# Performance work log

Measured on AMD Instinct MI355X. Metric: run time of the kernel, lower is better.

Reference implementation:

```python
import jax, jax.numpy as jnp
import numpy as np

B, T_IN, T_OUT = 32, 512, 800
N_MEL, ENC, ARNN, DRNN, PRE, ATT, LOCF, LOCK = 80, 512, 1024, 1024, 256, 128, 32, 31


def setup_inputs() -> dict:
    key = jax.random.key(0)
    ks = jax.random.split(key, 24)
    s = 0.02
    d = {
        'memory': jax.random.normal(ks[0], (B, T_IN, ENC), jnp.float32),
        'decoder_inputs': jax.random.normal(ks[1], (B, N_MEL, T_OUT), jnp.float32),
        'prenet_w1': jax.random.normal(ks[2], (PRE, N_MEL)) * s,
        'prenet_w2': jax.random.normal(ks[3], (PRE, PRE)) * s,
        'att_rnn_wih': jax.random.normal(ks[4], (4 * ARNN, PRE + ENC)) * s,
        'att_rnn_whh': jax.random.normal(ks[5], (4 * ARNN, ARNN)) * s,
        'att_rnn_bih': jnp.zeros((4 * ARNN,)),
        'att_rnn_bhh': jnp.zeros((4 * ARNN,)),
        'q_w': jax.random.normal(ks[6], (ATT, ARNN)) * s,
        'mem_w': jax.random.normal(ks[7], (ATT, ENC)) * s,
        'v_w': jax.random.normal(ks[8], (1, ATT)) * s,
        'loc_conv_w': jax.random.normal(ks[9], (LOCF, 2, LOCK)) * s,
        'loc_lin_w': jax.random.normal(ks[10], (ATT, LOCF)) * s,
        'dec_rnn_wih': jax.random.normal(ks[11], (4 * DRNN, ARNN + ENC)) * s,
        'dec_rnn_whh': jax.random.normal(ks[12], (4 * DRNN, DRNN)) * s,
        'dec_rnn_bih': jnp.zeros((4 * DRNN,)),
        'dec_rnn_bhh': jnp.zeros((4 * DRNN,)),
        'proj_w': jax.random.normal(ks[13], (N_MEL, DRNN + ENC)) * s,
        'proj_b': jnp.zeros((N_MEL,)),
        'gate_w': jax.random.normal(ks[14], (1, DRNN + ENC)) * s,
        'gate_b': jnp.zeros((1,)),
    }
    lengths = jax.random.randint(ks[15], (B,), T_IN // 2, T_IN + 1)
    d['memory_lengths'] = lengths.at[0].set(T_IN)  # ensure max length spans memory
    return d


def _lstm_cell(x, h, c, wih, whh, bih, bhh):
    z = x @ wih.T + bih + h @ whh.T + bhh
    i, f, g, o = jnp.split(z, 4, axis=-1)
    c = jax.nn.sigmoid(f) * c + jax.nn.sigmoid(i) * jnp.tanh(g)
    h = jax.nn.sigmoid(o) * jnp.tanh(c)
    return h, c


def reference(memory, decoder_inputs, prenet_w1, prenet_w2,
              att_rnn_wih, att_rnn_whh, att_rnn_bih, att_rnn_bhh,
              q_w, mem_w, v_w, loc_conv_w, loc_lin_w,
              dec_rnn_wih, dec_rnn_whh, dec_rnn_bih, dec_rnn_bhh,
              proj_w, proj_b, gate_w, gate_b, memory_lengths):
    # teacher-forced inputs: go frame + first T_OUT-1 mel frames -> [T_OUT, B, N_MEL]
    frames = jnp.transpose(decoder_inputs, (2, 0, 1))  # [T_OUT, B, N_MEL]
    dec_in = jnp.concatenate([jnp.zeros((1, B, N_MEL), memory.dtype), frames[:-1]], 0)
    # prenet (dropout omitted for deterministic reference)
    x = jax.nn.relu(dec_in @ prenet_w1.T)
    pren = jax.nn.relu(x @ prenet_w2.T)  # [T_OUT, B, PRE]

    pmem = memory @ mem_w.T  # [B, T_IN, ATT]
    valid = jnp.arange(T_IN)[None, :] < memory_lengths[:, None]  # [B, T_IN]

    def step(carry, dec_t):
        ah, ac, dh, dc, aw, awc, actx = carry
        cell_in = jnp.concatenate([dec_t, actx], -1)
        ah, ac = _lstm_cell(cell_in, ah, ac, att_rnn_wih, att_rnn_whh, att_rnn_bih, att_rnn_bhh)
        # location-sensitive attention
        cat = jnp.stack([aw, awc], axis=1)  # [B, 2, T_IN]
        loc = jax.lax.conv_general_dilated(cat, loc_conv_w, (1,), 'SAME',
                                           dimension_numbers=('NCH', 'OIH', 'NCH'))  # [B, LOCF, T_IN]
        loc = jnp.einsum('bct,ac->bta', loc, loc_lin_w)  # [B, T_IN, ATT]
        pq = (ah @ q_w.T)[:, None, :]  # [B, 1, ATT]
        energies = jnp.einsum('bta,a->bt', jnp.tanh(pq + loc + pmem), v_w[0])
        energies = jnp.where(valid, energies, -1e9)
        aw = jax.nn.softmax(energies, axis=1)
        actx = jnp.einsum('bt,btd->bd', aw, memory)
        awc = awc + aw
        din = jnp.concatenate([ah, actx], -1)
        dh, dc = _lstm_cell(din, dh, dc, dec_rnn_wih, dec_rnn_whh, dec_rnn_bih, dec_rnn_bhh)
        dhac = jnp.concatenate([dh, actx], -1)
        mel = dhac @ proj_w.T + proj_b  # [B, N_MEL]
        gate = (dhac @ gate_w.T + gate_b)[:, 0]  # [B]
        return (ah, ac, dh, dc, aw, awc, actx), (mel, gate, aw)

    z = lambda *s: jnp.zeros(s, memory.dtype)
    carry0 = (z(B, ARNN), z(B, ARNN), z(B, DRNN), z(B, DRNN), z(B, T_IN), z(B, T_IN), z(B, ENC))
    _, (mels, gates, aligns) = jax.lax.scan(step, carry0, pren)
    mel_outputs = jnp.transpose(mels, (1, 2, 0))      # [B, N_MEL, T_OUT]
    gate_outputs = jnp.transpose(gates, (1, 0))       # [B, T_OUT]
    alignments = jnp.transpose(aligns, (1, 0, 2))     # [B, T_OUT, T_IN]
    return mel_outputs, gate_outputs, alignments
```

## Files before the change

### kernel.cpp

```cpp
#include <hip/hip_runtime.h>
#include <cstddef>


constexpr size_t WT_ATT = 0;
constexpr size_t WT_DEC = 7340032;
constexpr size_t PREN_O = 17825792;
constexpr size_t PMEMT  = 24379392;
constexpr size_t W1T    = 26476544;
constexpr size_t W2T    = 26497024;
constexpr size_t QWT    = 26562560;
constexpr size_t PWT    = 26693632;
constexpr size_t MEMWT  = 26841088;
constexpr size_t ZDEC0  = 26906624;
constexpr size_t ZDEC1  = 27037696;
constexpr size_t AH_O   = 27185152;
constexpr size_t AC_O   = 27217920;
constexpr size_t DH_O   = 27250688;
constexpr size_t DC_O   = 27283456;
constexpr size_t AWC_O  = 27316224;
constexpr size_t ACTX_O = 27348992;
constexpr size_t ENER_O = 27381760;
constexpr size_t LOC_O  = 27398144;
constexpr size_t BAR_O  = 27922432;

constexpr size_t MEL_OUT = 0;
constexpr size_t GATE_OUT = 2048000;
constexpr size_t ALIGN_OUT = 2073600;

__device__ __forceinline__ float* zatt_ptr(float* ws, int b) {
  return ws + (b < 21 ? (size_t)W1T + (size_t)b * 4096
                      : (size_t)MEMWT + (size_t)(b - 21) * 4096);
}

__device__ __forceinline__ float gload(const float* p_) {
  return __hip_atomic_load(p_, __ATOMIC_RELAXED, __HIP_MEMORY_SCOPE_AGENT);
}
__device__ __forceinline__ void gstore(float* p_, float v) {
  __hip_atomic_store(p_, v, __ATOMIC_RELAXED, __HIP_MEMORY_SCOPE_AGENT);
}

__device__ __forceinline__ void gsync(float* ws, unsigned& epoch) {
  unsigned* cnt = (unsigned*)(ws + BAR_O);
  unsigned* rel = (unsigned*)(ws + BAR_O) + 128;
  __syncthreads();
  const int tid = threadIdx.x, bid = blockIdx.x;
  ++epoch;
  if (tid == 0)
    __hip_atomic_fetch_add(&cnt[(bid & 31) * 4], 1u, __ATOMIC_RELAXED,
                           __HIP_MEMORY_SCOPE_AGENT);
  if (bid == 0) {
    if (tid < 64) {
      const unsigned tgt = epoch * 24u;
      bool done;
      do {
        unsigned v = (tid < 32) ? __hip_atomic_load(&cnt[tid * 4], __ATOMIC_RELAXED,
                                                    __HIP_MEMORY_SCOPE_AGENT)
                                : tgt;
        done = v >= tgt;
        if (!done) __builtin_amdgcn_s_sleep(2);
      } while (__ballot(done) != ~0ull);
      for (int rr = tid; rr < 768; rr += 64)
        __hip_atomic_store(&rel[rr * 4], epoch, __ATOMIC_RELAXED,
                           __HIP_MEMORY_SCOPE_AGENT);
    }
  } else if (tid == 0) {
    while (__hip_atomic_load(&rel[bid * 4], __ATOMIC_RELAXED,
                             __HIP_MEMORY_SCOPE_AGENT) < epoch)
      __builtin_amdgcn_s_sleep(4);
  }
  __syncthreads();
}

__device__ __forceinline__ float sigf(float x) {
  float cx = fminf(fmaxf(x, -30.f), 30.f);
  return 1.f / (1.f + __expf(-cx));
}
__device__ __forceinline__ float tanh_f(float x) {
  float cx = fminf(fmaxf(x, -15.f), 15.f);
  float e = __expf(2.f * cx);
  return (e - 1.f) / (e + 1.f);
}

__device__ __forceinline__ void fused2(
    float* __restrict__ ws,
    const float* __restrict__ XA, const int sA, const int ncA,
    const float* __restrict__ XB, const int sB,
    const int nc, const float* __restrict__ WB,
    const int mode, const int g, const int b0, const int t,
    const float* __restrict__ bih, const float* __restrict__ bhh,
    float* __restrict__ cst, float* __restrict__ d0,
    const int tid, float* __restrict__ sm) {
  float* Xs = sm;
  float* Ws = sm + 2560;
  const int cg = tid & 7, bg = (tid >> 3) & 1, ks = tid >> 4;
  float acc[4][8];
#pragma unroll
  for (int ci = 0; ci < 4; ++ci)
#pragma unroll
    for (int bi = 0; bi < 8; ++bi) acc[ci][bi] = 0.f;

  const int kloc = tid & 127, brow = tid >> 7;
  float px[8];
  float4 pw[4];
  {
#pragma unroll
    for (int i = 0; i < 8; ++i)
      px[i] = gload(XA + (size_t)(brow + 2 * i) * sA + kloc);
  }
#pragma unroll
  for (int j = 0; j < 4; ++j)
    pw[j] = *(const float4*)(WB + (size_t)tid * 4 + j * 1024);

#pragma unroll 1
  for (int c = 0; c < nc; ++c) {
    __syncthreads();
#pragma unroll
    for (int i = 0; i < 8; ++i) Xs[kloc * 20 + brow + 2 * i] = px[i];
#pragma unroll
    for (int j = 0; j < 4; ++j) {
      const int ff = tid + 256 * j;
      *(float4*)(Ws + (ff >> 3) * 36 + (ff & 7) * 4) = pw[j];
    }
    __syncthreads();
    if (c + 1 < nc) {
      const int c2 = c + 1;
      const bool inA = c2 < ncA;
      const float* base = inA ? XA : XB;
      const int st = inA ? sA : sB;
      const int ko = (inA ? c2 : c2 - ncA) * 128;
#pragma unroll
      for (int i = 0; i < 8; ++i)
        px[i] = gload(base + (size_t)(brow + 2 * i) * st + ko + kloc);
      const float* wb2 = WB + (size_t)c2 * 4096 + (size_t)tid * 4;
#pragma unroll
      for (int j = 0; j < 4; ++j) pw[j] = *(const float4*)(wb2 + j * 1024);
    }
#pragma unroll
    for (int i = 0; i < 8; ++i) {
      const int k = i * 16 + ks;
      const float4 wA = *(const float4*)(Ws + k * 36 + cg * 4);
      const float4 xA = *(const float4*)(Xs + k * 20 + bg * 8);
      const float4 xBv = *(const float4*)(Xs + k * 20 + bg * 8 + 4);
      const float wr[4] = {wA.x, wA.y, wA.z, wA.w};
      const float xr[8] = {xA.x, xA.y, xA.z, xA.w, xBv.x, xBv.y, xBv.z, xBv.w};
#pragma unroll
      for (int ci = 0; ci < 4; ++ci)
#pragma unroll
        for (int bi = 0; bi < 8; ++bi)
          acc[ci][bi] = fmaf(wr[ci], xr[bi], acc[ci][bi]);
    }
  }
#pragma unroll
  for (int ci = 0; ci < 4; ++ci)
#pragma unroll
    for (int bi = 0; bi < 8; ++bi) {
      float v = acc[ci][bi];
      v += __shfl_xor(v, 16);
      v += __shfl_xor(v, 32);
      acc[ci][bi] = v;
    }
  __syncthreads();
  float* red = sm;
  float* zs = sm + 2560;
  const int lane = tid & 63, wv = tid >> 6;
  if (lane < 16) {
#pragma unroll
    for (int ci = 0; ci < 4; ++ci)
#pragma unroll
      for (int bi = 0; bi < 8; ++bi)
        red[((bg * 8 + bi) * 32 + cg * 4 + ci) * 5 + wv] = acc[ci][bi];
  }
  __syncthreads();
#pragma unroll
  for (int m = 0; m < 2; ++m) {
    const int o = tid + 256 * m;
    zs[o] = red[o * 5] + red[o * 5 + 1] + red[o * 5 + 2] + red[o * 5 + 3];
  }
  __syncthreads();
  if (mode <= 2) {
#pragma unroll
    for (int m = 0; m < 2; ++m) {
      const int o = tid + 256 * m, bb = o >> 5, cp = o & 31, b = b0 + bb;
      float* dst = (mode == 2)
                       ? (zatt_ptr(ws, b) + (size_t)g * 32 + cp)
                       : (ws + (mode ? ZDEC1 : ZDEC0) + (size_t)b * 4096 +
                          (size_t)g * 32 + cp);
      gstore(dst, zs[o]);
    }
    return;
  }
  if (tid < 128) {
    const int bb = tid & 15, jj = tid >> 4;
    const int j = g * 8 + jj;
    const int b = b0 + bb;
    float za0 = 0.f, za1 = 0.f, za2 = 0.f, za3 = 0.f;
    if (mode == 3) {
      if (t > 0) {
        const float* zp = zatt_ptr(ws, b) + (size_t)g * 32 + jj;
        za0 = gload(zp);
        za1 = gload(zp + 8);
        za2 = gload(zp + 16);
        za3 = gload(zp + 24);
      }
    } else {
      const float* z0 = ws + ZDEC0 + (size_t)b * 4096 + (size_t)g * 32 + jj;
      const float* z1 = ws + ZDEC1 + (size_t)b * 4096 + (size_t)g * 32 + jj;
      za0 = gload(z0) + gload(z1);
      za1 = gload(z0 + 8) + gload(z1 + 8);
      za2 = gload(z0 + 16) + gload(z1 + 16);
      za3 = gload(z0 + 24) + gload(z1 + 24);
    }
    const float zi = zs[bb * 32 + jj] + za0 + bih[j] + bhh[j];
    const float zf = zs[bb * 32 + 8 + jj] + za1 + bih[1024 + j] + bhh[1024 + j];
    const float zg = zs[bb * 32 + 16 + jj] + za2 + bih[2048 + j] + bhh[2048 + j];
    const float zo = zs[bb * 32 + 24 + jj] + za3 + bih[3072 + j] + bhh[3072 + j];
    const float cp = cst[(size_t)b * 1024 + j];
    const float ct = sigf(zf) * cp + sigf(zi) * tanh_f(zg);
    const float ho = sigf(zo) * tanh_f(ct);
    cst[(size_t)b * 1024 + j] = ct;
    gstore(d0 + (size_t)b * 1024 + j, ho);
  }
}

__global__ __launch_bounds__(256) void k_small(
    const float* __restrict__ w1, const float* __restrict__ w2,
    const float* __restrict__ qw, const float* __restrict__ memw,
    const float* __restrict__ projw, const float* __restrict__ gatew,
    float* __restrict__ ws) {
  size_t i = (size_t)blockIdx.x * 256 + threadIdx.x;
  if (i < 20480) { size_t j = i & 255, m = i >> 8; ws[W1T + m * 256 + j] = w1[j * 80 + m]; return; }
  i -= 20480;
  if (i < 65536) { size_t j = i & 255, k = i >> 8; ws[W2T + k * 256 + j] = w2[j * 256 + k]; return; }
  i -= 65536;
  if (i < 131072) { size_t j = i & 127, k = i >> 7; ws[QWT + k * 128 + j] = qw[j * 1024 + k]; return; }
  i -= 131072;
  if (i < 65536) { size_t a = i & 127, e = i >> 7; ws[MEMWT + e * 128 + a] = memw[a * 512 + e]; return; }
  i -= 65536;
  if (i < 147456) {
    size_t o = i % 96, k = i / 96;
    float v = 0.f;
    if (o < 80) v = projw[o * 1536 + k];
    else if (o == 80) v = gatew[k];
    ws[PWT + k * 96 + o] = v;
  }
}

__device__ __forceinline__ size_t att_out(int gcol, int kout) {
  const int gate = gcol >> 10, g = (gcol & 1023) >> 3, jj = gcol & 7;
  return WT_ATT + ((size_t)g * 1792 + kout) * 32 + gate * 8 + jj;
}
__device__ __forceinline__ size_t dec_out(int gcol, int kout) {
  const int gate = gcol >> 10, g = (gcol & 1023) >> 3, jj = gcol & 7;
  return WT_DEC + ((size_t)g * 2560 + kout) * 32 + gate * 8 + jj;
}
__global__ __launch_bounds__(256) void k_tr_a_wih(const float* __restrict__ w,
                                                  float* __restrict__ ws) {
  const int i = blockIdx.x * 256 + threadIdx.x;
  const int gcol = i / 768, k = i - gcol * 768;
  ws[att_out(gcol, k)] = w[i];
}
__global__ __launch_bounds__(256) void k_tr_a_whh(const float* __restrict__ w,
                                                  float* __restrict__ ws) {
  const int i = blockIdx.x * 256 + threadIdx.x;
  const int gcol = i >> 10, kin = i & 1023;
  ws[att_out(gcol, 768 + kin)] = w[i];
}
__global__ __launch_bounds__(256) void k_tr_d_wih(const float* __restrict__ w,
                                                  float* __restrict__ ws) {
  const int i = blockIdx.x * 256 + threadIdx.x;
  const int gcol = i / 1536, kin = i - gcol * 1536;
  const int kout = (kin < 1024) ? kin : kin + 1024;
  ws[dec_out(gcol, kout)] = w[i];
}
__global__ __launch_bounds__(256) void k_tr_d_whh(const float* __restrict__ w,
                                                  float* __restrict__ ws) {
  const int i = blockIdx.x * 256 + threadIdx.x;
  const int gcol = i >> 10, kin = i & 1023;
  ws[dec_out(gcol, 1024 + kin)] = w[i];
}

__global__ __launch_bounds__(256) void k_prenet(const float* __restrict__ din,
                                                float* __restrict__ ws) {
  __shared__ float h1[8][257];
  const int tg = blockIdx.x, b = blockIdx.y, j = threadIdx.x;
  float acc[8] = {0, 0, 0, 0, 0, 0, 0, 0};
  for (int m = 0; m < 80; ++m) {
    const float w = ws[W1T + m * 256 + j];
#pragma unroll
    for (int q = 0; q < 8; ++q) {
      const int t = tg * 8 + q;
      const float x = (t > 0) ? din[((size_t)b * 80 + m) * 800 + (t - 1)] : 0.f;
      acc[q] = fmaf(x, w, acc[q]);
    }
  }
#pragma unroll
  for (int q = 0; q < 8; ++q) h1[q][j] = fmaxf(acc[q], 0.f);
  __syncthreads();
  float a2[8] = {0, 0, 0, 0, 0, 0, 0, 0};
  for (int k = 0; k < 256; ++k) {
    const float w = ws[W2T + k * 256 + j];
#pragma unroll
    for (int q = 0; q < 8; ++q) a2[q] = fmaf(h1[q][k], w, a2[q]);
  }
#pragma unroll
  for (int q = 0; q < 8; ++q) {
    const int t = tg * 8 + q;
    ws[PREN_O + ((size_t)t * 32 + b) * 256 + j] = fmaxf(a2[q], 0.f);
  }
}

__global__ __launch_bounds__(256) void k_pmem(const float* __restrict__ mem,
                                              float* __restrict__ ws) {
  __shared__ float mt[16 * 516];
  const int b = blockIdx.x, tc = blockIdx.y, tid = threadIdx.x;
  const int ti0 = tc * 16;
  for (int i = tid; i < 16 * 128; i += 256) {
    const int r = i >> 7, c = i & 127;
    *(float4*)(mt + r * 516 + c * 4) =
        *(const float4*)(mem + ((size_t)b * 512 + ti0 + r) * 512 + c * 4);
  }
  __syncthreads();
  const int a = tid & 127, th = tid >> 7;
  float acc[8] = {0, 0, 0, 0, 0, 0, 0, 0};
  for (int e = 0; e < 512; ++e) {
    const float w = ws[MEMWT + (size_t)e * 128 + a];
#pragma unroll
    for (int q = 0; q < 8; ++q) acc[q] = fmaf(w, mt[(th * 8 + q) * 516 + e], acc[q]);
  }
#pragma unroll
  for (int q = 0; q < 8; ++q)
    ws[PMEMT + ((size_t)b * 128 + a) * 512 + ti0 + th * 8 + q] = acc[q];
}

struct TP {
  const float *mem, *abih, *abhh, *lconv, *llw, *vw, *dbih, *dbhh, *projb, *gateb;
  const int* lens;
  float* ws;
  float* out;
};

__global__ __launch_bounds__(256, 3) void taco_main(TP p) {
  __shared__ float smem[7168];
  float* const ws = p.ws;
  unsigned epoch = 0;
  const int bid = blockIdx.x, tid = threadIdx.x;
  const int grp = bid >> 8, r = bid & 255;

#pragma unroll 1
  for (int t = 0; t <= 800; ++t) {
    const int par = t & 1, nxt = (t + 1) & 1, prv = (t - 1) & 1;
    if (grp == 0) {
      if (t < 800) {
        const int g = r >> 1, hh = r & 1, b0 = hh * 16;
        fused2(ws,
               ws + PREN_O + ((size_t)t * 32 + b0) * 256, 256, 2,
               ws + ACTX_O + (size_t)prv * 16384 + (size_t)b0 * 512, 512,
               6, ws + WT_ATT + (size_t)g * 1792 * 32,
               3, g, b0, t, p.abih, p.abhh, ws + AC_O, ws + AH_O,
               tid, smem);
      }
    } else if (grp == 1) {
      if (t > 0) {
        const int g = r >> 1, hh = r & 1, b0 = hh * 16;
        fused2(ws,
               ws + ACTX_O + (size_t)prv * 16384 + (size_t)b0 * 512, 512, 4,
               nullptr, 0,
               4, ws + WT_DEC + (size_t)g * 2560 * 32 + (size_t)2048 * 32,
               4, g, b0, t, p.dbih, p.dbhh, ws + DC_O, ws + DH_O,
               tid, smem);
      }
    }
    gsync(ws, epoch);

    if (t < 800) {
      if (grp == 0) {
        const int b = r >> 3, q8 = r & 7;
        float* sa = smem;
        float* sloc = smem + 1024;
        float* pqp = smem + 3136;
        float* pq = smem + 3392;
        float* sme = smem + 3520;
#pragma unroll
        for (int i = 0; i < 4; ++i)
          sa[tid + 256 * i] = gload(ws + AH_O + (size_t)b * 1024 + tid + 256 * i);
#pragma unroll
        for (int ii = 0; ii < 8; ++ii) {
          const int flat = tid + 256 * ii;
          sloc[(flat >> 5) * 33 + (flat & 31)] =
              gload(ws + LOC_O + (size_t)b * 16384 + (size_t)q8 * 2048 + flat);
        }
        __syncthreads();
        {
          const int j = tid & 127, kh = tid >> 7;
          const float* qb = ws + QWT + (size_t)kh * 512 * 128 + j;
          const float* ab = sa + kh * 512;
          float a0 = 0, a1 = 0, a2 = 0, a3 = 0;
          for (int k = 0; k < 512; k += 4) {
            a0 = fmaf(qb[(size_t)k * 128], ab[k], a0);
            a1 = fmaf(qb[(size_t)(k + 1) * 128], ab[k + 1], a1);
            a2 = fmaf(qb[(size_t)(k + 2) * 128], ab[k + 2], a2);
            a3 = fmaf(qb[(size_t)(k + 3) * 128], ab[k + 3], a3);
          }
          pqp[tid] = (a0 + a1) + (a2 + a3);
        }
        __syncthreads();
        if (tid < 128) pq[tid] = pqp[tid] + pqp[128 + tid];
        __syncthreads();
        const int ti_l = tid & 63, th = tid >> 6;
        float lr[32];
#pragma unroll
        for (int f = 0; f < 32; ++f) lr[f] = sloc[ti_l * 33 + f];
        const float* pmb = ws + PMEMT + (size_t)b * 65536 +
                           (size_t)(th * 32) * 512 + q8 * 64 + ti_l;
        float acc_e = 0;
#pragma unroll 2
        for (int a0 = 0; a0 < 32; ++a0) {
          const int a = th * 32 + a0;
          float s = pq[a] + pmb[(size_t)a0 * 512];
          const float* la = p.llw + a * 32;
#pragma unroll
          for (int f = 0; f < 32; ++f) s = fmaf(lr[f], la[f], s);
          acc_e = fmaf(p.vw[a], tanh_f(s), acc_e);
        }
        sme[tid] = acc_e;
        __syncthreads();
        if (tid < 64) {
          const int ti = q8 * 64 + tid;
          const float e = sme[tid] + sme[64 + tid] + sme[128 + tid] + sme[192 + tid];
          gstore(ws + ENER_O + (size_t)b * 512 + ti, (ti < p.lens[b]) ? e : -1e9f);
        }
      } else if (grp == 1) {
        const int g = r >> 1, hh = r & 1, b0 = hh * 16;
        fused2(ws, ws + AH_O + (size_t)b0 * 1024, 1024, 8, nullptr, 0, 8,
               ws + WT_DEC + (size_t)g * 2560 * 32,
               0, g, b0, t, nullptr, nullptr, nullptr, nullptr,
               tid, smem);
      } else {
        const int g = r >> 1, hh = r & 1, b0 = hh * 16;
        fused2(ws, ws + DH_O + (size_t)b0 * 1024, 1024, 8, nullptr, 0, 8,
               ws + WT_DEC + (size_t)g * 2560 * 32 + (size_t)1024 * 32,
               1, g, b0, t, nullptr, nullptr, nullptr, nullptr,
               tid, smem);
      }
    }
    gsync(ws, epoch);

    if (grp == 1 && t < 800) {
      const int b = r >> 3, dc8 = r & 7;
      float* se = smem;
      float* red = smem + 512;
      float* sp = smem + 768;
      float* sc = smem + 1280;
      float* saw = smem + 1536;
      float* sawh = smem + 1664;
      float* slc = smem + 1792;
      se[tid] = gload(ws + ENER_O + (size_t)b * 512 + tid);
      se[256 + tid] = gload(ws + ENER_O + (size_t)b * 512 + 256 + tid);
      for (int i = tid; i < 1984; i += 256) slc[i] = p.lconv[i];
      __syncthreads();
      red[tid] = fmaxf(se[tid], se[256 + tid]);
      __syncthreads();
      for (int s = 128; s > 0; s >>= 1) {
        if (tid < s) red[tid] = fmaxf(red[tid], red[tid + s]);
        __syncthreads();
      }
      const float mx = red[0];
      __syncthreads();
      const float p0 = __expf(se[tid] - mx), p1 = __expf(se[256 + tid] - mx);
      sp[tid] = p0;
      sp[256 + tid] = p1;
      red[tid] = p0 + p1;
      __syncthreads();
      for (int s = 128; s > 0; s >>= 1) {
        if (tid < s) red[tid] += red[tid + s];
        __syncthreads();
      }
      const float inv = 1.f / red[0];
      const int tseg = tid >> 6, dl = tid & 63;
      const int base = dc8 * 64;
      const float* mrow = p.mem + ((size_t)b * 512 + tseg * 128) * 512 + base + dl;
      float ca = 0, cb = 0;
      for (int i = 0; i < 128; i += 2) {
        ca = fmaf(sp[tseg * 128 + i], mrow[(size_t)i * 512], ca);
        cb = fmaf(sp[tseg * 128 + i + 1], mrow[(size_t)(i + 1) * 512], cb);
      }
      sc[tid] = ca + cb;
      for (int i = tid; i < 95; i += 256) {
        const int x = base - 15 + i;
        const bool ok = (unsigned)x < 512u;
        const float awx = ok ? sp[x] * inv : 0.f;
        saw[i] = awx;
        sawh[i] = awx + (ok ? gload(ws + AWC_O + (size_t)par * 16384 +
                                    (size_t)b * 512 + x)
                            : 0.f);
      }
      __syncthreads();
      if (tid < 64) {
        const float v = (sc[tid] + sc[64 + tid] + sc[128 + tid] + sc[192 + tid]) * inv;
        const int dd = base + tid;
        gstore(ws + ACTX_O + (size_t)par * 16384 + (size_t)b * 512 + dd, v);
        gstore(ws + AWC_O + (size_t)nxt * 16384 + (size_t)b * 512 + dd,
               sawh[15 + tid]);
        p.out[ALIGN_OUT + ((size_t)b * 800 + t) * 512 + dd] = sp[dd] * inv;
      }
      if (t + 1 < 800) {
        const int f = tid & 31, tig = tid >> 5;
#pragma unroll 1
        for (int tt = 0; tt < 8; ++tt) {
          const int til = tig + tt * 8;
          float a2 = 0;
#pragma unroll
          for (int k2 = 0; k2 < 31; ++k2) a2 = fmaf(saw[til + k2], slc[f * 62 + k2], a2);
#pragma unroll
          for (int k2 = 0; k2 < 31; ++k2)
            a2 = fmaf(sawh[til + k2], slc[f * 62 + 31 + k2], a2);
          gstore(ws + LOC_O + (size_t)b * 16384 + (size_t)(base + til) * 32 + f, a2);
        }
      }
    } else if (grp == 2 && t + 1 < 800) {
      const int g = r >> 1, hh = r & 1, b0 = hh * 16;
      fused2(ws, ws + AH_O + (size_t)b0 * 1024, 1024, 8, nullptr, 0, 8,
             ws + WT_ATT + (size_t)g * 1792 * 32 + (size_t)768 * 32,
             2, g, b0, t, nullptr, nullptr, nullptr, nullptr,
             tid, smem);
    } else if (grp == 0 && r < 32 && t > 0) {
      const int b = r;
      float* sx = smem;
      float* sred = smem + 1536;
#pragma unroll
      for (int i = 0; i < 6; ++i) {
        const int flat = tid + 256 * i;
        sx[flat] = (flat < 1024)
                       ? gload(ws + DH_O + (size_t)b * 1024 + flat)
                       : gload(ws + ACTX_O + (size_t)prv * 16384 + (size_t)b * 512 +
                               (flat - 1024));
      }
      __syncthreads();
      float p0 = 0.f, p1 = 0.f, p2 = 0.f, p3 = 0.f;
      const int o = tid / 3, ks2 = tid - o * 3;
      if (o < 81) {
        const float* wcol = ws + PWT + o;
        const int k0 = ks2 * 512;
        for (int k = k0; k < k0 + 512; k += 4) {
          p0 = fmaf(sx[k], wcol[(size_t)k * 96], p0);
          p1 = fmaf(sx[k + 1], wcol[(size_t)(k + 1) * 96], p1);
          p2 = fmaf(sx[k + 2], wcol[(size_t)(k + 2) * 96], p2);
          p3 = fmaf(sx[k + 3], wcol[(size_t)(k + 3) * 96], p3);
        }
      }
      sred[tid] = (p0 + p1) + (p2 + p3);
      __syncthreads();
      if (tid < 81) {
        float ssum = sred[tid * 3] + sred[tid * 3 + 1] + sred[tid * 3 + 2];
        ssum += (tid < 80) ? p.projb[tid] : p.gateb[0];
        if (tid < 80)
          p.out[MEL_OUT + ((size_t)b * 80 + tid) * 800 + (t - 1)] = ssum;
        else
          p.out[GATE_OUT + (size_t)b * 800 + (t - 1)] = ssum;
      }
    }
    gsync(ws, epoch);
  }
}

extern "C" void kernel_launch(void* const* d_in, const int* in_sizes, int n_in,
                              void* d_out, int out_size, void* d_ws, size_t ws_size,
                              hipStream_t stream) {
  (void)in_sizes; (void)n_in; (void)out_size; (void)ws_size;
  const float* mem = (const float*)d_in[0];
  const float* decin = (const float*)d_in[1];
  const float* w1 = (const float*)d_in[2];
  const float* w2 = (const float*)d_in[3];
  const float* awih = (const float*)d_in[4];
  const float* awhh = (const float*)d_in[5];
  const float* abih = (const float*)d_in[6];
  const float* abhh = (const float*)d_in[7];
  const float* qw = (const float*)d_in[8];
  const float* memw = (const float*)d_in[9];
  const float* vw = (const float*)d_in[10];
  const float* lconv = (const float*)d_in[11];
  const float* llw = (const float*)d_in[12];
  const float* dwih = (const float*)d_in[13];
  const float* dwhh = (const float*)d_in[14];
  const float* dbih = (const float*)d_in[15];
  const float* dbhh = (const float*)d_in[16];
  const float* projw = (const float*)d_in[17];
  const float* projb = (const float*)d_in[18];
  const float* gatew = (const float*)d_in[19];
  const float* gateb = (const float*)d_in[20];
  const int* lens = (const int*)d_in[21];
  float* ws = (float*)d_ws;
  float* out = (float*)d_out;

  hipMemsetAsync(ws + ZDEC0, 0, 278528 * sizeof(float), stream);
  hipMemsetAsync(ws + AH_O, 0, 737280 * sizeof(float), stream);
  hipMemsetAsync(ws + BAR_O, 0, 4224 * sizeof(unsigned), stream);

  k_small<<<1680, 256, 0, stream>>>(w1, w2, qw, memw, projw, gatew, ws);
  k_tr_a_wih<<<12288, 256, 0, stream>>>(awih, ws);
  k_tr_a_whh<<<16384, 256, 0, stream>>>(awhh, ws);
  k_tr_d_wih<<<24576, 256, 0, stream>>>(dwih, ws);
  k_tr_d_whh<<<16384, 256, 0, stream>>>(dwhh, ws);
  k_prenet<<<dim3(100, 32), 256, 0, stream>>>(decin, ws);
  k_pmem<<<dim3(32, 32), 256, 0, stream>>>(mem, ws);

  TP tp{mem, abih, abhh, lconv, llw, vw, dbih, dbhh, projb, gateb, lens, ws, out};
  taco_main<<<768, 256, 0, stream>>>(tp);
}
```

Measured before the change: 156.5 ms.

## Rebalance persistent kernel onto 512 blocks and split decoder Whh matvec

Shrinks the persistent grid from 768 to 512 blocks (launch bounds now 2 per SIMD) and redistributes work across the phases between grid barriers. The decoder hidden-state matvec is split into two halves: one runs alongside the energy computation and the other follows the softmax, accumulating into the same buffer. The mel/gate projection is now a two-way partial sum combined in the next phase. The aim is to balance per-phase load and use fewer blocks per barrier. The cost is extra global accumulation traffic and more work per block.

```diff
diff --git a/kernel.cpp b/kernel.cpp
--- a/kernel.cpp
+++ b/kernel.cpp
@@ -11,8 +11,9 @@
 constexpr size_t QWT    = 26562560;
 constexpr size_t PWT    = 26693632;
 constexpr size_t MEMWT  = 26841088;
-constexpr size_t ZDEC0  = 26906624;
-constexpr size_t ZDEC1  = 27037696;
+constexpr size_t ZDA_O  = 26906624;
+constexpr size_t ZDH_O  = 27037696;
+constexpr size_t PP_O   = 27168768;
 constexpr size_t AH_O   = 27185152;
 constexpr size_t AC_O   = 27217920;
 constexpr size_t DH_O   = 27250688;
@@ -46,25 +47,25 @@
   const int tid = threadIdx.x, bid = blockIdx.x;
   ++epoch;
   if (tid == 0)
-    __hip_atomic_fetch_add(&cnt[(bid & 31) * 4], 1u, __ATOMIC_RELAXED,
+    __hip_atomic_fetch_add(&cnt[(bid & 15) * 8], 1u, __ATOMIC_RELAXED,
                            __HIP_MEMORY_SCOPE_AGENT);
   if (bid == 0) {
     if (tid < 64) {
-      const unsigned tgt = epoch * 24u;
+      const unsigned tgt = epoch * 32u;
       bool done;
       do {
-        unsigned v = (tid < 32) ? __hip_atomic_load(&cnt[tid * 4], __ATOMIC_RELAXED,
+        unsigned v = (tid < 16) ? __hip_atomic_load(&cnt[tid * 8], __ATOMIC_RELAXED,
                                                     __HIP_MEMORY_SCOPE_AGENT)
                                 : tgt;
         done = v >= tgt;
         if (!done) __builtin_amdgcn_s_sleep(2);
       } while (__ballot(done) != ~0ull);
-      for (int rr = tid; rr < 768; rr += 64)
-        __hip_atomic_store(&rel[rr * 4], epoch, __ATOMIC_RELAXED,
+      for (int rr = tid; rr < 512; rr += 64)
+        __hip_atomic_store(&rel[rr * 8], epoch, __ATOMIC_RELAXED,
                            __HIP_MEMORY_SCOPE_AGENT);
     }
   } else if (tid == 0) {
-    while (__hip_atomic_load(&rel[bid * 4], __ATOMIC_RELAXED,
+    while (__hip_atomic_load(&rel[bid * 8], __ATOMIC_RELAXED,
                              __HIP_MEMORY_SCOPE_AGENT) < epoch)
       __builtin_amdgcn_s_sleep(4);
   }
@@ -177,15 +178,17 @@
     zs[o] = red[o * 5] + red[o * 5 + 1] + red[o * 5 + 2] + red[o * 5 + 3];
   }
   __syncthreads();
-  if (mode <= 2) {
+  if (mode <= 2 || mode == 5) {
 #pragma unroll
     for (int m = 0; m < 2; ++m) {
       const int o = tid + 256 * m, bb = o >> 5, cp = o & 31, b = b0 + bb;
-      float* dst = (mode == 2)
-                       ? (zatt_ptr(ws, b) + (size_t)g * 32 + cp)
-                       : (ws + (mode ? ZDEC1 : ZDEC0) + (size_t)b * 4096 +
-                          (size_t)g * 32 + cp);
-      gstore(dst, zs[o]);
+      float* dst;
+      if (mode == 2) dst = zatt_ptr(ws, b) + (size_t)g * 32 + cp;
+      else if (mode == 0) dst = ws + ZDA_O + (size_t)b * 4096 + (size_t)g * 32 + cp;
+      else dst = ws + ZDH_O + (size_t)b * 4096 + (size_t)g * 32 + cp;
+      float v = zs[o];
+      if (mode == 5) v += gload(dst);
+      gstore(dst, v);
     }
     return;
   }
@@ -203,8 +206,8 @@
         za3 = gload(zp + 24);
       }
     } else {
-      const float* z0 = ws + ZDEC0 + (size_t)b * 4096 + (size_t)g * 32 + jj;
-      const float* z1 = ws + ZDEC1 + (size_t)b * 4096 + (size_t)g * 32 + jj;
+      const float* z0 = ws + ZDA_O + (size_t)b * 4096 + (size_t)g * 32 + jj;
+      const float* z1 = ws + ZDH_O + (size_t)b * 4096 + (size_t)g * 32 + jj;
       za0 = gload(z0) + gload(z1);
       za1 = gload(z0 + 8) + gload(z1 + 8);
       za2 = gload(z0 + 16) + gload(z1 + 16);
@@ -339,19 +342,18 @@
   float* out;
 };
 
-__global__ __launch_bounds__(256, 3) void taco_main(TP p) {
+__global__ __launch_bounds__(256, 2) void taco_main(TP p) {
   __shared__ float smem[7168];
   float* const ws = p.ws;
   unsigned epoch = 0;
   const int bid = blockIdx.x, tid = threadIdx.x;
-  const int grp = bid >> 8, r = bid & 255;
 
 #pragma unroll 1
   for (int t = 0; t <= 800; ++t) {
     const int par = t & 1, nxt = (t + 1) & 1, prv = (t - 1) & 1;
-    if (grp == 0) {
+    if (bid < 256) {
       if (t < 800) {
-        const int g = r >> 1, hh = r & 1, b0 = hh * 16;
+        const int g = bid >> 1, b0 = (bid & 1) * 16;
         fused2(ws,
                ws + PREN_O + ((size_t)t * 32 + b0) * 256, 256, 2,
                ws + ACTX_O + (size_t)prv * 16384 + (size_t)b0 * 512, 512,
@@ -359,9 +361,9 @@
                3, g, b0, t, p.abih, p.abhh, ws + AC_O, ws + AH_O,
                tid, smem);
       }
-    } else if (grp == 1) {
+    } else {
       if (t > 0) {
-        const int g = r >> 1, hh = r & 1, b0 = hh * 16;
+        const int rd = bid - 256, g = rd >> 1, b0 = (rd & 1) * 16;
         fused2(ws,
                ws + ACTX_O + (size_t)prv * 16384 + (size_t)b0 * 512, 512, 4,
                nullptr, 0,
@@ -372,191 +374,218 @@
     }
     gsync(ws, epoch);
 
-    if (t < 800) {
-      if (grp == 0) {
-        const int b = r >> 3, q8 = r & 7;
-        float* sa = smem;
-        float* sloc = smem + 1024;
-        float* pqp = smem + 3136;
-        float* pq = smem + 3392;
-        float* sme = smem + 3520;
-#pragma unroll
-        for (int i = 0; i < 4; ++i)
-          sa[tid + 256 * i] = gload(ws + AH_O + (size_t)b * 1024 + tid + 256 * i);
-#pragma unroll
-        for (int ii = 0; ii < 8; ++ii) {
-          const int flat = tid + 256 * ii;
-          sloc[(flat >> 5) * 33 + (flat & 31)] =
-              gload(ws + LOC_O + (size_t)b * 16384 + (size_t)q8 * 2048 + flat);
-        }
-        __syncthreads();
+    if (bid < 256) {
+      if (t < 800) {
         {
-          const int j = tid & 127, kh = tid >> 7;
-          const float* qb = ws + QWT + (size_t)kh * 512 * 128 + j;
-          const float* ab = sa + kh * 512;
-          float a0 = 0, a1 = 0, a2 = 0, a3 = 0;
-          for (int k = 0; k < 512; k += 4) {
-            a0 = fmaf(qb[(size_t)k * 128], ab[k], a0);
-            a1 = fmaf(qb[(size_t)(k + 1) * 128], ab[k + 1], a1);
-            a2 = fmaf(qb[(size_t)(k + 2) * 128], ab[k + 2], a2);
-            a3 = fmaf(qb[(size_t)(k + 3) * 128], ab[k + 3], a3);
+          const int b = bid >> 3, q8 = bid & 7;
+          float* sa = smem;
+          float* sloc = smem + 1024;
+          float* pqp = smem + 3136;
+          float* pq = smem + 3392;
+          float* sme = smem + 3520;
+#pragma unroll
+          for (int i = 0; i < 4; ++i)
+            sa[tid + 256 * i] = gload(ws + AH_O + (size_t)b * 1024 + tid + 256 * i);
+#pragma unroll
+          for (int ii = 0; ii < 8; ++ii) {
+            const int flat = tid + 256 * ii;
+            sloc[(flat >> 5) * 33 + (flat & 31)] =
+                gload(ws + LOC_O + (size_t)b * 16384 + (size_t)q8 * 2048 + flat);
           }
-          pqp[tid] = (a0 + a1) + (a2 + a3);
-        }
-        __syncthreads();
-        if (tid < 128) pq[tid] = pqp[tid] + pqp[128 + tid];
-        __syncthreads();
-        const int ti_l = tid & 63, th = tid >> 6;
-        float lr[32];
-#pragma unroll
-        for (int f = 0; f < 32; ++f) lr[f] = sloc[ti_l * 33 + f];
-        const float* pmb = ws + PMEMT + (size_t)b * 65536 +
-                           (size_t)(th * 32) * 512 + q8 * 64 + ti_l;
-        float acc_e = 0;
+          __syncthreads();
+          {
+            const int j = tid & 127, kh = tid >> 7;
+            const float* qb = ws + QWT + (size_t)kh * 512 * 128 + j;
+            const float* ab = sa + kh * 512;
+            float a0 = 0, a1 = 0, a2 = 0, a3 = 0;
+            for (int k = 0; k < 512; k += 4) {
+              a0 = fmaf(qb[(size_t)k * 128], ab[k], a0);
+              a1 = fmaf(qb[(size_t)(k + 1) * 128], ab[k + 1], a1);
+              a2 = fmaf(qb[(size_t)(k + 2) * 128], ab[k + 2], a2);
+              a3 = fmaf(qb[(size_t)(k + 3) * 128], ab[k + 3], a3);
+            }
+            pqp[tid] = (a0 + a1) + (a2 + a3);
+          }
+          __syncthreads();
+          if (tid < 128) pq[tid] = pqp[tid] + pqp[128 + tid];
+          __syncthreads();
+          const int ti_l = tid & 63, th = tid >> 6;
+          float lr[32];
+#pragma unroll
+          for (int f = 0; f < 32; ++f) lr[f] = sloc[ti_l * 33 + f];
+          const float* pmb = ws + PMEMT + (size_t)b * 65536 +
+                             (size_t)(th * 32) * 512 + q8 * 64 + ti_l;
+          float acc_e = 0;
 #pragma unroll 2
-        for (int a0 = 0; a0 < 32; ++a0) {
-          const int a = th * 32 + a0;
-          float s = pq[a] + pmb[(size_t)a0 * 512];
-          const float* la = p.llw + a * 32;
-#pragma unroll
-          for (int f = 0; f < 32; ++f) s = fmaf(lr[f], la[f], s);
-          acc_e = fmaf(p.vw[a], tanh_f(s), acc_e);
-        }
-        sme[tid] = acc_e;
-        __syncthreads();
-        if (tid < 64) {
-          const int ti = q8 * 64 + tid;
-          const float e = sme[tid] + sme[64 + tid] + sme[128 + tid] + sme[192 + tid];
-          gstore(ws + ENER_O + (size_t)b * 512 + ti, (ti < p.lens[b]) ? e : -1e9f);
-        }
-      } else if (grp == 1) {
-        const int g = r >> 1, hh = r & 1, b0 = hh * 16;
+          for (int a0 = 0; a0 < 32; ++a0) {
+            const int a = th * 32 + a0;
+            float s = pq[a] + pmb[(size_t)a0 * 512];
+            const float* la = p.llw + a * 32;
+#pragma unroll
+            for (int f = 0; f < 32; ++f) s = fmaf(lr[f], la[f], s);
+            acc_e = fmaf(p.vw[a], tanh_f(s), acc_e);
+          }
+          sme[tid] = acc_e;
+          __syncthreads();
+          if (tid < 64) {
+            const int ti = q8 * 64 + tid;
+            const float e = sme[tid] + sme[64 + tid] + sme[128 + tid] + sme[192 + tid];
+            gstore(ws + ENER_O + (size_t)b * 512 + ti, (ti < p.lens[b]) ? e : -1e9f);
+          }
+        }
+        {
+          const int g = bid >> 1, b0 = (bid & 1) * 16;
+          fused2(ws, ws + DH_O + (size_t)b0 * 1024, 1024, 3, nullptr, 0, 3,
+                 ws + WT_DEC + (size_t)g * 2560 * 32 + (size_t)1024 * 32,
+                 1, g, b0, t, nullptr, nullptr, nullptr, nullptr,
+                 tid, smem);
+        }
+      }
+    } else {
+      const int rd = bid - 256;
+      if (t + 1 < 800) {
+        const int g = rd >> 1, b0 = (rd & 1) * 16;
+        fused2(ws, ws + AH_O + (size_t)b0 * 1024, 1024, 8, nullptr, 0, 8,
+               ws + WT_ATT + (size_t)g * 1792 * 32 + (size_t)768 * 32,
+               2, g, b0, t, nullptr, nullptr, nullptr, nullptr,
+               tid, smem);
+      }
+      if (t > 0 && rd < 64) {
+        const int b = rd >> 1, h = rd & 1;
+        float* sx = smem;
+        float* sred = smem + 768;
+        __syncthreads();
+#pragma unroll
+        for (int i = 0; i < 3; ++i) {
+          const int flat = tid + 256 * i;
+          const int gk = h * 768 + flat;
+          sx[flat] = (gk < 1024)
+                         ? gload(ws + DH_O + (size_t)b * 1024 + gk)
+                         : gload(ws + ACTX_O + (size_t)prv * 16384 +
+                                 (size_t)b * 512 + (gk - 1024));
+        }
+        __syncthreads();
+        float p0 = 0.f, p1 = 0.f, p2 = 0.f, p3 = 0.f;
+        const int o = tid / 3, ks2 = tid - o * 3;
+        if (o < 81) {
+          const float* wcol = ws + PWT + (size_t)(h * 768) * 96 + o;
+          const int k0 = ks2 * 256;
+          for (int k = k0; k < k0 + 256; k += 4) {
+            p0 = fmaf(sx[k], wcol[(size_t)k * 96], p0);
+            p1 = fmaf(sx[k + 1], wcol[(size_t)(k + 1) * 96], p1);
+            p2 = fmaf(sx[k + 2], wcol[(size_t)(k + 2) * 96], p2);
+            p3 = fmaf(sx[k + 3], wcol[(size_t)(k + 3) * 96], p3);
+          }
+        }
+        sred[tid] = (p0 + p1) + (p2 + p3);
+        __syncthreads();
+        if (tid < 81) {
+          const float v = sred[tid * 3] + sred[tid * 3 + 1] + sred[tid * 3 + 2];
+          gstore(ws + PP_O + ((size_t)b * 2 + h) * 81 + tid, v);
+        }
+      }
+    }
+    gsync(ws, epoch);
+
+    if (bid < 256) {
+      if (t < 800) {
+        const int g = bid >> 1, b0 = (bid & 1) * 16;
         fused2(ws, ws + AH_O + (size_t)b0 * 1024, 1024, 8, nullptr, 0, 8,
                ws + WT_DEC + (size_t)g * 2560 * 32,
                0, g, b0, t, nullptr, nullptr, nullptr, nullptr,
                tid, smem);
-      } else {
-        const int g = r >> 1, hh = r & 1, b0 = hh * 16;
-        fused2(ws, ws + DH_O + (size_t)b0 * 1024, 1024, 8, nullptr, 0, 8,
-               ws + WT_DEC + (size_t)g * 2560 * 32 + (size_t)1024 * 32,
-               1, g, b0, t, nullptr, nullptr, nullptr, nullptr,
+      }
+      if (t > 0 && bid < 32 && tid < 81) {
+        const int b = bid;
+        float v = gload(ws + PP_O + (size_t)b * 2 * 81 + tid) +
+                  gload(ws + PP_O + ((size_t)b * 2 + 1) * 81 + tid);
+        v += (tid < 80) ? p.projb[tid] : p.gateb[0];
+        if (tid < 80)
+          p.out[MEL_OUT + ((size_t)b * 80 + tid) * 800 + (t - 1)] = v;
+        else
+          p.out[GATE_OUT + (size_t)b * 800 + (t - 1)] = v;
+      }
+    } else if (t < 800) {
+      const int rd = bid - 256;
+      {
+        const int b = rd >> 3, dc8 = rd & 7;
+        float* se = smem;
+        float* red = smem + 512;
+        float* sp = smem + 768;
+        float* sc = smem + 1280;
+        float* saw = smem + 1536;
+        float* sawh = smem + 1664;
+        float* slc = smem + 1792;
+        se[tid] = gload(ws + ENER_O + (size_t)b * 512 + tid);
+        se[256 + tid] = gload(ws + ENER_O + (size_t)b * 512 + 256 + tid);
+        for (int i = tid; i < 1984; i += 256) slc[i] = p.lconv[i];
+        __syncthreads();
+        red[tid] = fmaxf(se[tid], se[256 + tid]);
+        __syncthreads();
+        for (int s = 128; s > 0; s >>= 1) {
+          if (tid < s) red[tid] = fmaxf(red[tid], red[tid + s]);
+          __syncthreads();
+        }
+        const float mx = red[0];
+        __syncthreads();
+        const float p0 = __expf(se[tid] - mx), p1 = __expf(se[256 + tid] - mx);
+        sp[tid] = p0;
+        sp[256 + tid] = p1;
+        red[tid] = p0 + p1;
+        __syncthreads();
+        for (int s = 128; s > 0; s >>= 1) {
+          if (tid < s) red[tid] += red[tid + s];
+          __syncthreads();
+        }
+        const float inv = 1.f / red[0];
+        const int tseg = tid >> 6, dl = tid & 63;
+        const int base = dc8 * 64;
+        const float* mrow = p.mem + ((size_t)b * 512 + tseg * 128) * 512 + base + dl;
+        float ca = 0, cb = 0;
+        for (int i = 0; i < 128; i += 2) {
+          ca = fmaf(sp[tseg * 128 + i], mrow[(size_t)i * 512], ca);
+          cb = fmaf(sp[tseg * 128 + i + 1], mrow[(size_t)(i + 1) * 512], cb);
+        }
+        sc[tid] = ca + cb;
+        for (int i = tid; i < 95; i += 256) {
+          const int x = base - 15 + i;
+          const bool ok = (unsigned)x < 512u;
+          const float awx = ok ? sp[x] * inv : 0.f;
+          saw[i] = awx;
+          sawh[i] = awx + (ok ? gload(ws + AWC_O + (size_t)par * 16384 +
+                                      (size_t)b * 512 + x)
+                              : 0.f);
+        }
+        __syncthreads();
+        if (tid < 64) {
+          const float v = (sc[tid] + sc[64 + tid] + sc[128 + tid] + sc[192 + tid]) * inv;
+          const int dd = base + tid;
+          gstore(ws + ACTX_O + (size_t)par * 16384 + (size_t)b * 512 + dd, v);
+          gstore(ws + AWC_O + (size_t)nxt * 16384 + (size_t)b * 512 + dd,
+                 sawh[15 + tid]);
+          p.out[ALIGN_OUT + ((size_t)b * 800 + t) * 512 + dd] = sp[dd] * inv;
+        }
+        if (t + 1 < 800) {
+          const int f = tid & 31, tig = tid >> 5;
+#pragma unroll 1
+          for (int tt = 0; tt < 8; ++tt) {
+            const int til = tig + tt * 8;
+            float a2 = 0;
+#pragma unroll
+            for (int k2 = 0; k2 < 31; ++k2) a2 = fmaf(saw[til + k2], slc[f * 62 + k2], a2);
+#pragma unroll
+            for (int k2 = 0; k2 < 31; ++k2)
+              a2 = fmaf(sawh[til + k2], slc[f * 62 + 31 + k2], a2);
+            gstore(ws + LOC_O + (size_t)b * 16384 + (size_t)(base + til) * 32 + f, a2);
+          }
+        }
+      }
+      {
+        const int g = rd >> 1, b0 = (rd & 1) * 16;
+        fused2(ws, ws + DH_O + (size_t)b0 * 1024 + 384, 1024, 5, nullptr, 0, 5,
+               ws + WT_DEC + (size_t)g * 2560 * 32 + (size_t)1408 * 32,
+               5, g, b0, t, nullptr, nullptr, nullptr, nullptr,
                tid, smem);
-      }
-    }
-    gsync(ws, epoch);
-
-    if (grp == 1 && t < 800) {
-      const int b = r >> 3, dc8 = r & 7;
-      float* se = smem;
-      float* red = smem + 512;
-      float* sp = smem + 768;
-      float* sc = smem + 1280;
-      float* saw = smem + 1536;
-      float* sawh = smem + 1664;
-      float* slc = smem + 1792;
-      se[tid] = gload(ws + ENER_O + (size_t)b * 512 + tid);
-      se[256 + tid] = gload(ws + ENER_O + (size_t)b * 512 + 256 + tid);
-      for (int i = tid; i < 1984; i += 256) slc[i] = p.lconv[i];
-      __syncthreads();
-      red[tid] = fmaxf(se[tid], se[256 + tid]);
-      __syncthreads();
-      for (int s = 128; s > 0; s >>= 1) {
-        if (tid < s) red[tid] = fmaxf(red[tid], red[tid + s]);
-        __syncthreads();
-      }
-      const float mx = red[0];
-      __syncthreads();
-      const float p0 = __expf(se[tid] - mx), p1 = __expf(se[256 + tid] - mx);
-      sp[tid] = p0;
-      sp[256 + tid] = p1;
-      red[tid] = p0 + p1;
-      __syncthreads();
-      for (int s = 128; s > 0; s >>= 1) {
-        if (tid < s) red[tid] += red[tid + s];
-        __syncthreads();
-      }
-      const float inv = 1.f / red[0];
-      const int tseg = tid >> 6, dl = tid & 63;
-      const int base = dc8 * 64;
-      const float* mrow = p.mem + ((size_t)b * 512 + tseg * 128) * 512 + base + dl;
-      float ca = 0, cb = 0;
-      for (int i = 0; i < 128; i += 2) {
-        ca = fmaf(sp[tseg * 128 + i], mrow[(size_t)i * 512], ca);
-        cb = fmaf(sp[tseg * 128 + i + 1], mrow[(size_t)(i + 1) * 512], cb);
-      }
-      sc[tid] = ca + cb;
-      for (int i = tid; i < 95; i += 256) {
-        const int x = base - 15 + i;
-        const bool ok = (unsigned)x < 512u;
-        const float awx = ok ? sp[x] * inv : 0.f;
-        saw[i] = awx;
-        sawh[i] = awx + (ok ? gload(ws + AWC_O + (size_t)par * 16384 +
-                                    (size_t)b * 512 + x)
-                            : 0.f);
-      }
-      __syncthreads();
-      if (tid < 64) {
-        const float v = (sc[tid] + sc[64 + tid] + sc[128 + tid] + sc[192 + tid]) * inv;
-        const int dd = base + tid;
-        gstore(ws + ACTX_O + (size_t)par * 16384 + (size_t)b * 512 + dd, v);
-        gstore(ws + AWC_O + (size_t)nxt * 16384 + (size_t)b * 512 + dd,
-               sawh[15 + tid]);
-        p.out[ALIGN_OUT + ((size_t)b * 800 + t) * 512 + dd] = sp[dd] * inv;
-      }
-      if (t + 1 < 800) {
-        const int f = tid & 31, tig = tid >> 5;
-#pragma unroll 1
-        for (int tt = 0; tt < 8; ++tt) {
-          const int til = tig + tt * 8;
-          float a2 = 0;
-#pragma unroll
-          for (int k2 = 0; k2 < 31; ++k2) a2 = fmaf(saw[til + k2], slc[f * 62 + k2], a2);
-#pragma unroll
-          for (int k2 = 0; k2 < 31; ++k2)
-            a2 = fmaf(sawh[til + k2], slc[f * 62 + 31 + k2], a2);
-          gstore(ws + LOC_O + (size_t)b * 16384 + (size_t)(base + til) * 32 + f, a2);
-        }
-      }
-    } else if (grp == 2 && t + 1 < 800) {
-      const int g = r >> 1, hh = r & 1, b0 = hh * 16;
-      fused2(ws, ws + AH_O + (size_t)b0 * 1024, 1024, 8, nullptr, 0, 8,
-             ws + WT_ATT + (size_t)g * 1792 * 32 + (size_t)768 * 32,
-             2, g, b0, t, nullptr, nullptr, nullptr, nullptr,
-             tid, smem);
-    } else if (grp == 0 && r < 32 && t > 0) {
-      const int b = r;
-      float* sx = smem;
-      float* sred = smem + 1536;
-#pragma unroll
-      for (int i = 0; i < 6; ++i) {
-        const int flat = tid + 256 * i;
-        sx[flat] = (flat < 1024)
-                       ? gload(ws + DH_O + (size_t)b * 1024 + flat)
-                       : gload(ws + ACTX_O + (size_t)prv * 16384 + (size_t)b * 512 +
-                               (flat - 1024));
-      }
-      __syncthreads();
-      float p0 = 0.f, p1 = 0.f, p2 = 0.f, p3 = 0.f;
-      const int o = tid / 3, ks2 = tid - o * 3;
-      if (o < 81) {
-        const float* wcol = ws + PWT + o;
-        const int k0 = ks2 * 512;
-        for (int k = k0; k < k0 + 512; k += 4) {
-          p0 = fmaf(sx[k], wcol[(size_t)k * 96], p0);
-          p1 = fmaf(sx[k + 1], wcol[(size_t)(k + 1) * 96], p1);
-          p2 = fmaf(sx[k + 2], wcol[(size_t)(k + 2) * 96], p2);
-          p3 = fmaf(sx[k + 3], wcol[(size_t)(k + 3) * 96], p3);
-        }
-      }
-      sred[tid] = (p0 + p1) + (p2 + p3);
-      __syncthreads();
-      if (tid < 81) {
-        float ssum = sred[tid * 3] + sred[tid * 3 + 1] + sred[tid * 3 + 2];
-        ssum += (tid < 80) ? p.projb[tid] : p.gateb[0];
-        if (tid < 80)
-          p.out[MEL_OUT + ((size_t)b * 80 + tid) * 800 + (t - 1)] = ssum;
-        else
-          p.out[GATE_OUT + (size_t)b * 800 + (t - 1)] = ssum;
       }
     }
     gsync(ws, epoch);
@@ -592,7 +621,7 @@
   float* ws = (float*)d_ws;
   float* out = (float*)d_out;
 
-  hipMemsetAsync(ws + ZDEC0, 0, 278528 * sizeof(float), stream);
+  hipMemsetAsync(ws + ZDA_O, 0, 278528 * sizeof(float), stream);
   hipMemsetAsync(ws + AH_O, 0, 737280 * sizeof(float), stream);
   hipMemsetAsync(ws + BAR_O, 0, 4224 * sizeof(unsigned), stream);
 
@@ -605,5 +634,5 @@
   k_pmem<<<dim3(32, 32), 256, 0, stream>>>(mem, ws);
 
   TP tp{mem, abih, abhh, lconv, llw, vw, dbih, dbhh, projb, gateb, lens, ws, out};
-  taco_main<<<768, 256, 0, stream>>>(tp);
-}
+  taco_main<<<512, 256, 0, stream>>>(tp);
+}
```

Result: slower. 180.1 ms (+15.1%).
